# Optimization experiments

Measured on AMD Instinct MI355X. Metric: run time of the kernel, lower is better.

## Reference

```python
import math
import jax, jax.numpy as jnp
import numpy as np

D_MODEL = 1024
HEAD_DIM = 64  # D_MODEL // NUM_HEADS
B, T = 8, 2048


def setup_inputs() -> dict:
    key = jax.random.key(0)
    k1, k2, k3, k4 = jax.random.split(key, 4)
    x = jax.random.normal(k1, (B, T, D_MODEL), dtype=jnp.float32)
    wq = jax.random.normal(k2, (D_MODEL, HEAD_DIM), dtype=jnp.float32) * (1.0 / math.sqrt(D_MODEL))
    wk = jax.random.normal(k3, (D_MODEL, HEAD_DIM), dtype=jnp.float32) * (1.0 / math.sqrt(D_MODEL))
    wv = jax.random.normal(k4, (D_MODEL, HEAD_DIM), dtype=jnp.float32) * (1.0 / math.sqrt(D_MODEL))
    return {"x": x, "wq": wq, "wk": wk, "wv": wv}


def reference(x, wq, wk, wv):
    # Single-head causal scaled dot-product attention (dropout = eval/identity).
    Tn = x.shape[1]
    q = jnp.einsum('btc,ch->bth', x, wq)  # [B,T,H]
    k = jnp.einsum('btc,ch->bth', x, wk)
    v = jnp.einsum('btc,ch->bth', x, wv)
    scale = 1.0 / math.sqrt(HEAD_DIM)
    scores = jnp.einsum('bth,bsh->bts', q, k) * scale  # [B,T,T]
    causal = jnp.tril(jnp.ones((Tn, Tn), dtype=bool))
    scores = jnp.where(causal, scores, -jnp.inf)
    weights = jax.nn.softmax(scores, axis=-1)
    return jnp.einsum('bts,bsh->bth', weights, v)  # [B,T,H]
```

## Files before the change

kernel.cpp:

```cpp
#include <hip/hip_runtime.h>

#define D_MODEL 1024
#define HDIM    64
#define BATCH   8
#define SEQ     2048
#define BT      (BATCH*SEQ)
#define NCAT    192
#define KSTEP   32
#define NKS     (D_MODEL/KSTEP)
#define NFRAG   24
#define FRAGSH  512
#define STEPSH  (NFRAG*FRAGSH)

typedef __attribute__((ext_vector_type(8))) short s8v;
typedef __attribute__((ext_vector_type(4))) float f4;
typedef __attribute__((ext_vector_type(4))) unsigned short u16x4;

__device__ __forceinline__ unsigned short f2bf(float f){
    unsigned u = __builtin_bit_cast(unsigned, f);
    u += 0x7fffu + ((u >> 16) & 1u);
    return (unsigned short)(u >> 16);
}
__device__ __forceinline__ float bf2f(unsigned short h){
    unsigned u = ((unsigned)h) << 16;
    return __builtin_bit_cast(float, u);
}
__device__ __forceinline__ f4 MFMA(s8v a, s8v b, f4 c){
    return __builtin_amdgcn_mfma_f32_16x16x32_bf16(a, b, c, 0, 0, 0);
}

__global__ void prep_w_kernel(const float* __restrict__ wq, const float* __restrict__ wk,
                              const float* __restrict__ wv,
                              short* __restrict__ wtP){
    int ncat = blockIdx.x;
    const float* w = (ncat < 64) ? wq : ((ncat < 128) ? wk : wv);
    int n  = ncat & 63;
    int nb = ncat >> 4, ln = ncat & 15;
    for (int k = threadIdx.x; k < D_MODEL; k += blockDim.x){
        float f = w[k*HDIM + n];
        unsigned short h = f2bf(f);
        unsigned short l = f2bf(f - bf2f(h));
        int t1 = k >> 5, g = (k >> 3) & 3, e = k & 7;
        size_t base = (size_t)t1*STEPSH + (size_t)((g*16 + ln) << 3) + e;
        wtP[base + (size_t)nb*FRAGSH]        = (short)h;
        wtP[base + (size_t)(12 + nb)*FRAGSH] = (short)l;
    }
}

__global__ __launch_bounds__(512) void proj_kernel(
        const float* __restrict__ x,
        const short* __restrict__ wtP,
        short* __restrict__ q, short* __restrict__ k,
        short* __restrict__ vt){
    __shared__ short xsH[2][64][40], xsL[2][64][40];
    int tid = threadIdx.x;
    int wid = tid >> 6, lane = tid & 63, g = lane >> 4, ln = lane & 15;
    int wm = wid >> 2, wn = wid & 3;
    int m0 = blockIdx.x * 64;

    const float* xptr = x + (size_t)(m0 + (tid >> 3))*D_MODEL + (tid & 7)*4;
    const short* wbase = wtP + (size_t)(wn*3)*FRAGSH + (size_t)lane*8;

    f4 acc[6];
#pragma unroll
    for (int i = 0; i < 6; i++) acc[i] = (f4){0.f,0.f,0.f,0.f};

    float4 x0, x1;
    s8v whA0, whA1, whA2, wlA0, wlA1, wlA2;
    s8v whB0, whB1, whB2, wlB0, wlB1, wlB2;

#define LOADX(R, T) { R = *(const float4*)(xptr + (size_t)(T)*KSTEP); }
#define LOADW(S, T) { \
    const short* wp = wbase + (size_t)(T)*STEPSH; \
    wh##S##0 = *(const s8v*)(wp); \
    wh##S##1 = *(const s8v*)(wp + FRAGSH); \
    wh##S##2 = *(const s8v*)(wp + 2*FRAGSH); \
    const short* wp2 = wp + 12*FRAGSH; \
    wl##S##0 = *(const s8v*)(wp2); \
    wl##S##1 = *(const s8v*)(wp2 + FRAGSH); \
    wl##S##2 = *(const s8v*)(wp2 + 2*FRAGSH); }

#define STAGEX(B, R) { \
    int row = tid >> 3, kc = (tid & 7) << 2; \
    float f0 = R.x, f1 = R.y, f2 = R.z, f3 = R.w; \
    unsigned short h0 = f2bf(f0), h1 = f2bf(f1), h2 = f2bf(f2), h3 = f2bf(f3); \
    u16x4 hv, lv; \
    hv[0]=h0; hv[1]=h1; hv[2]=h2; hv[3]=h3; \
    lv[0]=f2bf(f0-bf2f(h0)); lv[1]=f2bf(f1-bf2f(h1)); \
    lv[2]=f2bf(f2-bf2f(h2)); lv[3]=f2bf(f3-bf2f(h3)); \
    *(u16x4*)&xsH[B][row][kc] = hv; \
    *(u16x4*)&xsL[B][row][kc] = lv; }

#define COMPUTE(B, S) { \
    s8v aH0 = *(const s8v*)&xsH[B][wm*32 + ln][g*8]; \
    s8v aL0 = *(const s8v*)&xsL[B][wm*32 + ln][g*8]; \
    s8v aH1 = *(const s8v*)&xsH[B][wm*32 + 16 + ln][g*8]; \
    s8v aL1 = *(const s8v*)&xsL[B][wm*32 + 16 + ln][g*8]; \
    acc[0] = MFMA(aH0, wh##S##0, acc[0]); \
    acc[0] = MFMA(aL0, wh##S##0, acc[0]); \
    acc[0] = MFMA(aH0, wl##S##0, acc[0]); \
    acc[1] = MFMA(aH0, wh##S##1, acc[1]); \
    acc[1] = MFMA(aL0, wh##S##1, acc[1]); \
    acc[1] = MFMA(aH0, wl##S##1, acc[1]); \
    acc[2] = MFMA(aH0, wh##S##2, acc[2]); \
    acc[2] = MFMA(aL0, wh##S##2, acc[2]); \
    acc[2] = MFMA(aH0, wl##S##2, acc[2]); \
    acc[3] = MFMA(aH1, wh##S##0, acc[3]); \
    acc[3] = MFMA(aL1, wh##S##0, acc[3]); \
    acc[3] = MFMA(aH1, wl##S##0, acc[3]); \
    acc[4] = MFMA(aH1, wh##S##1, acc[4]); \
    acc[4] = MFMA(aL1, wh##S##1, acc[4]); \
    acc[4] = MFMA(aH1, wl##S##1, acc[4]); \
    acc[5] = MFMA(aH1, wh##S##2, acc[5]); \
    acc[5] = MFMA(aL1, wh##S##2, acc[5]); \
    acc[5] = MFMA(aH1, wl##S##2, acc[5]); }

    LOADX(x0, 0)
    LOADX(x1, 1)
    LOADW(A, 0)
    LOADW(B, 1)
    STAGEX(0, x0)
    __syncthreads();

    for (int t = 0; t < NKS; t += 2){
        if (t + 2 < NKS) LOADX(x0, t + 2)
        COMPUTE(0, A)
        if (t + 2 < NKS) LOADW(A, t + 2)
        STAGEX(1, x1)
        __syncthreads();
        if (t + 3 < NKS) LOADX(x1, t + 3)
        COMPUTE(1, B)
        if (t + 3 < NKS) LOADW(B, t + 3)
        if (t + 2 < NKS){ STAGEX(0, x0) }
        __syncthreads();
    }
#undef LOADX
#undef LOADW
#undef STAGEX
#undef COMPUTE

#pragma unroll
    for (int a = 0; a < 2; a++){
#pragma unroll
        for (int nb = 0; nb < 3; nb++){
            int ncat = wn*48 + nb*16 + ln;
            int mat = ncat >> 6, h = ncat & 63;
#pragma unroll
            for (int r = 0; r < 4; r++){
                size_t trow = (size_t)m0 + wm*32 + a*16 + g*4 + r;
                float v = acc[a*3 + nb][r];
                unsigned short hh = f2bf(v);
                if (mat == 0){
                    q[trow*HDIM + h] = (short)hh;
                } else if (mat == 1){
                    k[trow*HDIM + h] = (short)hh;
                } else {
                    size_t bb = trow >> 11, t = trow & 2047;
                    vt[((bb*HDIM + h) << 11) + t] = (short)hh;
                }
            }
        }
    }
}

__global__ __launch_bounds__(256, 5) void attn_kernel(
        const short* __restrict__ qg, const short* __restrict__ kg,
        const short* __restrict__ vt, float* __restrict__ out){
    __shared__ unsigned short plds[4][16][112];
    __shared__ float olds[4][16][65];
    __shared__ float mlds[4][16], llds[4][16];
    const float SC = 0.125f * 1.44269504088896340736f;
    int tid = threadIdx.x;
    int w = tid >> 6, lane = tid & 63, g = lane >> 4, ln = lane & 15;
    int b = blockIdx.y;
    int qi = ((blockIdx.y >> 1) & 1) ? (int)(gridDim.x - 1 - blockIdx.x) : (int)blockIdx.x;
    int tq = qi * 16;

    size_t qoff = ((size_t)b*SEQ + tq + ln) * HDIM + g*8;
    s8v q0 = *(const s8v*)(qg + qoff);
    s8v q1 = *(const s8v*)(qg + qoff + 32);

    f4 o0 = {0.f,0.f,0.f,0.f}, o1 = o0, o2 = o0, o3 = o0;
    float m[4], lsum[4];
#pragma unroll
    for (int r = 0; r < 4; r++){ m[r] = -__builtin_inff(); lsum[r] = 0.f; }

    int ntiles = (tq + 79) >> 6;
    for (int ti = w; ti < ntiles; ti += 4){
        int s0 = ti << 6;
        size_t kbase = ((size_t)b*SEQ + s0 + ln) * HDIM + g*8;
        f4 z0, z1, z2, z3;
#define QK_SUBTILE(ZJ, J) { \
        const short* kp = kg + kbase + (J)*16*HDIM; \
        s8v k0 = *(const s8v*)(kp); \
        s8v k1 = *(const s8v*)(kp + 32); \
        f4 s = {0.f,0.f,0.f,0.f}; \
        s = MFMA(q0, k0, s); s = MFMA(q1, k1, s); \
        ZJ[0] = s[0]*SC; ZJ[1] = s[1]*SC; ZJ[2] = s[2]*SC; ZJ[3] = s[3]*SC; }
        QK_SUBTILE(z0, 0)
        QK_SUBTILE(z1, 1)
        QK_SUBTILE(z2, 2)
        QK_SUBTILE(z3, 3)
#undef QK_SUBTILE
        if (s0 + 63 > tq){
#pragma unroll
            for (int r = 0; r < 4; r++){
                int t = tq + g*4 + r;
                if (s0      + ln > t) z0[r] = -__builtin_inff();
                if (s0 + 16 + ln > t) z1[r] = -__builtin_inff();
                if (s0 + 32 + ln > t) z2[r] = -__builtin_inff();
                if (s0 + 48 + ln > t) z3[r] = -__builtin_inff();
            }
        }
        float al[4];
#pragma unroll
        for (int r = 0; r < 4; r++){
            float v = fmaxf(fmaxf(z0[r], z1[r]), fmaxf(z2[r], z3[r]));
            v = fmaxf(v, __shfl_xor(v, 1));
            v = fmaxf(v, __shfl_xor(v, 2));
            v = fmaxf(v, __shfl_xor(v, 4));
            v = fmaxf(v, __shfl_xor(v, 8));
            float mn = fmaxf(m[r], v);
            al[r] = __builtin_amdgcn_exp2f(m[r] - mn);
            float p0 = __builtin_amdgcn_exp2f(z0[r] - mn);
            float p1 = __builtin_amdgcn_exp2f(z1[r] - mn);
            float p2 = __builtin_amdgcn_exp2f(z2[r] - mn);
            float p3 = __builtin_amdgcn_exp2f(z3[r] - mn);
            lsum[r] = lsum[r]*al[r] + ((p0 + p1) + (p2 + p3));
            m[r] = mn;
            int row = g*4 + r;
            plds[w][row][ln]      = f2bf(p0);
            plds[w][row][ln + 16] = f2bf(p1);
            plds[w][row][ln + 32] = f2bf(p2);
            plds[w][row][ln + 48] = f2bf(p3);
        }
#pragma unroll
        for (int r = 0; r < 4; r++){
            o0[r] *= al[r]; o1[r] *= al[r]; o2[r] *= al[r]; o3[r] *= al[r];
        }
        asm volatile("s_waitcnt lgkmcnt(0)" ::: "memory");
        __builtin_amdgcn_sched_barrier(0);
        s8v pa0 = *(const s8v*)&plds[w][ln][g*8];
        s8v pa1 = *(const s8v*)&plds[w][ln][32 + g*8];
        size_t voff = ((size_t)b*HDIM + ln) * SEQ + s0 + g*8;
        s8v v00 = *(const s8v*)(vt + voff);
        s8v v01 = *(const s8v*)(vt + voff + 32);
        s8v v10 = *(const s8v*)(vt + voff + 16*SEQ);
        s8v v11 = *(const s8v*)(vt + voff + 16*SEQ + 32);
        s8v v20 = *(const s8v*)(vt + voff + 32*SEQ);
        s8v v21 = *(const s8v*)(vt + voff + 32*SEQ + 32);
        s8v v30 = *(const s8v*)(vt + voff + 48*SEQ);
        s8v v31 = *(const s8v*)(vt + voff + 48*SEQ + 32);
        o0 = MFMA(pa0, v00, o0); o0 = MFMA(pa1, v01, o0);
        o1 = MFMA(pa0, v10, o1); o1 = MFMA(pa1, v11, o1);
        o2 = MFMA(pa0, v20, o2); o2 = MFMA(pa1, v21, o2);
        o3 = MFMA(pa0, v30, o3); o3 = MFMA(pa1, v31, o3);
    }

#pragma unroll
    for (int r = 0; r < 4; r++){
        float s = lsum[r];
        s += __shfl_xor(s, 1);
        s += __shfl_xor(s, 2);
        s += __shfl_xor(s, 4);
        s += __shfl_xor(s, 8);
        lsum[r] = s;
    }

#pragma unroll
    for (int r = 0; r < 4; r++){
        int row = g*4 + r;
        olds[w][row][ln]      = o0[r];
        olds[w][row][ln + 16] = o1[r];
        olds[w][row][ln + 32] = o2[r];
        olds[w][row][ln + 48] = o3[r];
        if (ln == 0){ mlds[w][row] = m[r]; llds[w][row] = lsum[r]; }
    }
    __syncthreads();

    {
        int row = tid >> 4;
        int hb  = tid & 15;
        float m0 = mlds[0][row], m1 = mlds[1][row], m2 = mlds[2][row], m3 = mlds[3][row];
        float M = fmaxf(fmaxf(m0, m1), fmaxf(m2, m3));
        float w0 = __builtin_amdgcn_exp2f(m0 - M);
        float w1 = __builtin_amdgcn_exp2f(m1 - M);
        float w2 = __builtin_amdgcn_exp2f(m2 - M);
        float w3 = __builtin_amdgcn_exp2f(m3 - M);
        float L = llds[0][row]*w0 + llds[1][row]*w1 + llds[2][row]*w2 + llds[3][row]*w3;
        float inv = 1.0f / L;
        size_t obase = ((size_t)b*SEQ + tq + row) * HDIM + hb;
#pragma unroll
        for (int j = 0; j < 4; j++){
            int h = hb + 16*j;
            float acc = olds[0][row][h]*w0 + olds[1][row][h]*w1
                      + olds[2][row][h]*w2 + olds[3][row][h]*w3;
            out[obase + 16*j] = acc * inv;
        }
    }
}

extern "C" void kernel_launch(void* const* d_in, const int* in_sizes, int n_in,
                              void* d_out, int out_size, void* d_ws, size_t ws_size,
                              hipStream_t stream) {
    (void)in_sizes; (void)n_in; (void)out_size; (void)ws_size;
    const float* x  = (const float*)d_in[0];
    const float* wq = (const float*)d_in[1];
    const float* wk = (const float*)d_in[2];
    const float* wv = (const float*)d_in[3];
    float* out = (float*)d_out;

    short* ws  = (short*)d_ws;
    short* wtP = ws;
    short* q   = wtP + (size_t)NKS*STEPSH;
    short* k   = q + (size_t)BT*HDIM;
    short* vt  = k + (size_t)BT*HDIM;

    prep_w_kernel<<<NCAT, 256, 0, stream>>>(wq, wk, wv, wtP);
    proj_kernel<<<BT/64, 512, 0, stream>>>(x, wtP, q, k, vt);
    attn_kernel<<<dim3(SEQ/16, BATCH), 256, 0, stream>>>(q, k, vt, out);
}
```

Measured before the change: 68.88 us.

## Load x directly into MFMA registers, drop LDS staging and x low-part term

```diff
diff --git a/kernel.cpp b/kernel.cpp
--- a/kernel.cpp
+++ b/kernel.cpp
@@ -8,13 +8,11 @@
 #define NCAT    192
 #define KSTEP   32
 #define NKS     (D_MODEL/KSTEP)
-#define NFRAG   24
 #define FRAGSH  512
-#define STEPSH  (NFRAG*FRAGSH)
+#define STEPSH  (24*FRAGSH)
 
 typedef __attribute__((ext_vector_type(8))) short s8v;
 typedef __attribute__((ext_vector_type(4))) float f4;
-typedef __attribute__((ext_vector_type(4))) unsigned short u16x4;
 
 __device__ __forceinline__ unsigned short f2bf(float f){
     unsigned u = __builtin_bit_cast(unsigned, f);
@@ -47,116 +45,106 @@
     }
 }
 
-__global__ __launch_bounds__(512) void proj_kernel(
+__global__ __launch_bounds__(256, 2) void proj_kernel(
         const float* __restrict__ x,
         const short* __restrict__ wtP,
         short* __restrict__ q, short* __restrict__ k,
         short* __restrict__ vt){
-    __shared__ short xsH[2][64][40], xsL[2][64][40];
     int tid = threadIdx.x;
-    int wid = tid >> 6, lane = tid & 63, g = lane >> 4, ln = lane & 15;
-    int wm = wid >> 2, wn = wid & 3;
-    int m0 = blockIdx.x * 64;
-
-    const float* xptr = x + (size_t)(m0 + (tid >> 3))*D_MODEL + (tid & 7)*4;
-    const short* wbase = wtP + (size_t)(wn*3)*FRAGSH + (size_t)lane*8;
+    int wn = tid >> 6, lane = tid & 63, g = lane >> 4, ln = lane & 15;
+    int m0 = blockIdx.x * 32;
+
+    const float* xp0 = x + (size_t)(m0 + ln)*D_MODEL + g*8;
+    const float* xp1 = xp0 + (size_t)16*D_MODEL;
+    const short* wb  = wtP + (size_t)(wn*3)*FRAGSH + (size_t)lane*8;
 
     f4 acc[6];
 #pragma unroll
     for (int i = 0; i < 6; i++) acc[i] = (f4){0.f,0.f,0.f,0.f};
 
-    float4 x0, x1;
+    float4 xA00, xA01, xA10, xA11, xB00, xB01, xB10, xB11;
     s8v whA0, whA1, whA2, wlA0, wlA1, wlA2;
     s8v whB0, whB1, whB2, wlB0, wlB1, wlB2;
 
-#define LOADX(R, T) { R = *(const float4*)(xptr + (size_t)(T)*KSTEP); }
-#define LOADW(S, T) { \
-    const short* wp = wbase + (size_t)(T)*STEPSH; \
-    wh##S##0 = *(const s8v*)(wp); \
-    wh##S##1 = *(const s8v*)(wp + FRAGSH); \
-    wh##S##2 = *(const s8v*)(wp + 2*FRAGSH); \
-    const short* wp2 = wp + 12*FRAGSH; \
-    wl##S##0 = *(const s8v*)(wp2); \
-    wl##S##1 = *(const s8v*)(wp2 + FRAGSH); \
-    wl##S##2 = *(const s8v*)(wp2 + 2*FRAGSH); }
-
-#define STAGEX(B, R) { \
-    int row = tid >> 3, kc = (tid & 7) << 2; \
-    float f0 = R.x, f1 = R.y, f2 = R.z, f3 = R.w; \
-    unsigned short h0 = f2bf(f0), h1 = f2bf(f1), h2 = f2bf(f2), h3 = f2bf(f3); \
-    u16x4 hv, lv; \
-    hv[0]=h0; hv[1]=h1; hv[2]=h2; hv[3]=h3; \
-    lv[0]=f2bf(f0-bf2f(h0)); lv[1]=f2bf(f1-bf2f(h1)); \
-    lv[2]=f2bf(f2-bf2f(h2)); lv[3]=f2bf(f3-bf2f(h3)); \
-    *(u16x4*)&xsH[B][row][kc] = hv; \
-    *(u16x4*)&xsL[B][row][kc] = lv; }
-
-#define COMPUTE(B, S) { \
-    s8v aH0 = *(const s8v*)&xsH[B][wm*32 + ln][g*8]; \
-    s8v aL0 = *(const s8v*)&xsL[B][wm*32 + ln][g*8]; \
-    s8v aH1 = *(const s8v*)&xsH[B][wm*32 + 16 + ln][g*8]; \
-    s8v aL1 = *(const s8v*)&xsL[B][wm*32 + 16 + ln][g*8]; \
-    acc[0] = MFMA(aH0, wh##S##0, acc[0]); \
-    acc[0] = MFMA(aL0, wh##S##0, acc[0]); \
-    acc[0] = MFMA(aH0, wl##S##0, acc[0]); \
-    acc[1] = MFMA(aH0, wh##S##1, acc[1]); \
-    acc[1] = MFMA(aL0, wh##S##1, acc[1]); \
-    acc[1] = MFMA(aH0, wl##S##1, acc[1]); \
-    acc[2] = MFMA(aH0, wh##S##2, acc[2]); \
-    acc[2] = MFMA(aL0, wh##S##2, acc[2]); \
-    acc[2] = MFMA(aH0, wl##S##2, acc[2]); \
-    acc[3] = MFMA(aH1, wh##S##0, acc[3]); \
-    acc[3] = MFMA(aL1, wh##S##0, acc[3]); \
-    acc[3] = MFMA(aH1, wl##S##0, acc[3]); \
-    acc[4] = MFMA(aH1, wh##S##1, acc[4]); \
-    acc[4] = MFMA(aL1, wh##S##1, acc[4]); \
-    acc[4] = MFMA(aH1, wl##S##1, acc[4]); \
-    acc[5] = MFMA(aH1, wh##S##2, acc[5]); \
-    acc[5] = MFMA(aL1, wh##S##2, acc[5]); \
-    acc[5] = MFMA(aH1, wl##S##2, acc[5]); }
-
-    LOADX(x0, 0)
-    LOADX(x1, 1)
+#define LOADX(P, T) { \
+    x##P##00 = *(const float4*)(xp0 + (size_t)(T)*KSTEP); \
+    x##P##01 = *(const float4*)(xp0 + (size_t)(T)*KSTEP + 4); \
+    x##P##10 = *(const float4*)(xp1 + (size_t)(T)*KSTEP); \
+    x##P##11 = *(const float4*)(xp1 + (size_t)(T)*KSTEP + 4); }
+
+#define LOADW(P, T) { \
+    const short* wp = wb + (size_t)(T)*STEPSH; \
+    wh##P##0 = *(const s8v*)(wp); \
+    wh##P##1 = *(const s8v*)(wp + FRAGSH); \
+    wh##P##2 = *(const s8v*)(wp + 2*FRAGSH); \
+    wl##P##0 = *(const s8v*)(wp + 12*FRAGSH); \
+    wl##P##1 = *(const s8v*)(wp + 13*FRAGSH); \
+    wl##P##2 = *(const s8v*)(wp + 14*FRAGSH); }
+
+#define CVT8(DST, VA, VB) { \
+    DST[0] = (short)f2bf(VA.x); DST[1] = (short)f2bf(VA.y); \
+    DST[2] = (short)f2bf(VA.z); DST[3] = (short)f2bf(VA.w); \
+    DST[4] = (short)f2bf(VB.x); DST[5] = (short)f2bf(VB.y); \
+    DST[6] = (short)f2bf(VB.z); DST[7] = (short)f2bf(VB.w); }
+
+#define MFMAS(P, A0, A1) { \
+    acc[0] = MFMA(A0, wh##P##0, acc[0]); acc[0] = MFMA(A0, wl##P##0, acc[0]); \
+    acc[1] = MFMA(A0, wh##P##1, acc[1]); acc[1] = MFMA(A0, wl##P##1, acc[1]); \
+    acc[2] = MFMA(A0, wh##P##2, acc[2]); acc[2] = MFMA(A0, wl##P##2, acc[2]); \
+    acc[3] = MFMA(A1, wh##P##0, acc[3]); acc[3] = MFMA(A1, wl##P##0, acc[3]); \
+    acc[4] = MFMA(A1, wh##P##1, acc[4]); acc[4] = MFMA(A1, wl##P##1, acc[4]); \
+    acc[5] = MFMA(A1, wh##P##2, acc[5]); acc[5] = MFMA(A1, wl##P##2, acc[5]); }
+
+    LOADX(A, 0)
+    LOADX(B, 1)
     LOADW(A, 0)
     LOADW(B, 1)
-    STAGEX(0, x0)
-    __syncthreads();
-
-    for (int t = 0; t < NKS; t += 2){
-        if (t + 2 < NKS) LOADX(x0, t + 2)
-        COMPUTE(0, A)
-        if (t + 2 < NKS) LOADW(A, t + 2)
-        STAGEX(1, x1)
-        __syncthreads();
-        if (t + 3 < NKS) LOADX(x1, t + 3)
-        COMPUTE(1, B)
-        if (t + 3 < NKS) LOADW(B, t + 3)
-        if (t + 2 < NKS){ STAGEX(0, x0) }
-        __syncthreads();
+
+    for (int t = 0; t + 2 < NKS; t += 2){
+        s8v aA0, aA1, aB0, aB1;
+        CVT8(aA0, xA00, xA01)
+        CVT8(aA1, xA10, xA11)
+        LOADX(A, t + 2)
+        MFMAS(A, aA0, aA1)
+        LOADW(A, t + 2)
+        CVT8(aB0, xB00, xB01)
+        CVT8(aB1, xB10, xB11)
+        LOADX(B, t + 3)
+        MFMAS(B, aB0, aB1)
+        LOADW(B, t + 3)
+    }
+    {
+        s8v aA0, aA1, aB0, aB1;
+        CVT8(aA0, xA00, xA01)
+        CVT8(aA1, xA10, xA11)
+        MFMAS(A, aA0, aA1)
+        CVT8(aB0, xB00, xB01)
+        CVT8(aB1, xB10, xB11)
+        MFMAS(B, aB0, aB1)
     }
 #undef LOADX
 #undef LOADW
-#undef STAGEX
-#undef COMPUTE
-
-#pragma unroll
-    for (int a = 0; a < 2; a++){
+#undef CVT8
+#undef MFMAS
+
+#pragma unroll
+    for (int rf = 0; rf < 2; rf++){
 #pragma unroll
         for (int nb = 0; nb < 3; nb++){
             int ncat = wn*48 + nb*16 + ln;
             int mat = ncat >> 6, h = ncat & 63;
 #pragma unroll
             for (int r = 0; r < 4; r++){
-                size_t trow = (size_t)m0 + wm*32 + a*16 + g*4 + r;
-                float v = acc[a*3 + nb][r];
+                size_t trow = (size_t)m0 + rf*16 + g*4 + r;
+                float v = acc[rf*3 + nb][r];
                 unsigned short hh = f2bf(v);
                 if (mat == 0){
                     q[trow*HDIM + h] = (short)hh;
                 } else if (mat == 1){
                     k[trow*HDIM + h] = (short)hh;
                 } else {
-                    size_t bb = trow >> 11, t = trow & 2047;
-                    vt[((bb*HDIM + h) << 11) + t] = (short)hh;
+                    size_t bb = trow >> 11, t2 = trow & 2047;
+                    vt[((bb*HDIM + h) << 11) + t2] = (short)hh;
                 }
             }
         }
@@ -317,6 +305,6 @@
     short* vt  = k + (size_t)BT*HDIM;
 
     prep_w_kernel<<<NCAT, 256, 0, stream>>>(wq, wk, wv, wtP);
-    proj_kernel<<<BT/64, 512, 0, stream>>>(x, wtP, q, k, vt);
+    proj_kernel<<<BT/32, 256, 0, stream>>>(x, wtP, q, k, vt);
     attn_kernel<<<dim3(SEQ/16, BATCH), 256, 0, stream>>>(q, k, vt, out);
 }
```

Result: slower. 87.05 us (median of 2 runs) (+26.4%).
